# Performance work log

Hardware: AMD Instinct MI355X
Metric: run time of the kernel (lower is better)

## Reference

```python
import jax, jax.numpy as jnp
import numpy as np

B, IDF, RES = 32, 64, 128
CDF, SRC_L, A_DIM = 768, 18, 100
QUERY_L = RES * RES


def setup_inputs() -> dict:
    key = jax.random.key(0)
    ks = jax.random.split(key, 5)
    inputs = jax.random.normal(ks[0], (B, IDF, RES, RES), dtype=jnp.float32)
    context = jax.random.normal(ks[1], (B, CDF, SRC_L), dtype=jnp.float32)
    conv_ctx_w = jax.random.normal(ks[2], (IDF, CDF), dtype=jnp.float32) * (1.0 / np.sqrt(CDF))
    conv_w = jax.random.normal(ks[3], (IDF,), dtype=jnp.float32) * (1.0 / np.sqrt(IDF))
    conv_b = jnp.zeros((1,), dtype=jnp.float32)
    fc_w = jax.random.normal(ks[4], (A_DIM, QUERY_L), dtype=jnp.float32) * (1.0 / np.sqrt(QUERY_L))
    fc_b = jnp.zeros((A_DIM,), dtype=jnp.float32)
    return {"inputs": inputs, "context": context, "conv_ctx_w": conv_ctx_w,
            "conv_w": conv_w, "conv_b": conv_b, "fc_w": fc_w, "fc_b": fc_b}


def reference(inputs, context, conv_ctx_w, conv_w, conv_b, fc_w, fc_b):
    b, idf, ih, iw = inputs.shape
    queryL = ih * iw
    # target: [b, idf, queryL]
    target = inputs.reshape(b, idf, queryL)
    # 1x1 conv on context (conv_context): [b, idf, sourceL]
    sourceT = jnp.einsum('ic,bcs->bis', conv_ctx_w, context)
    # attn scores: [b, queryL, sourceL]; softmax over sourceL (dim=1 on flattened view)
    attn = jnp.einsum('biq,bis->bqs', target, sourceT)
    attn = jax.nn.softmax(attn, axis=-1)
    # weighted context: [b, idf, queryL]
    wctx = jnp.einsum('bis,bqs->biq', sourceT, attn)
    # 1x1 conv to single channel (self.conv): [b, queryL]
    wctx = jnp.einsum('i,biq->bq', conv_w, wctx) + conv_b
    # att_fc: [b, a_dim]
    out = wctx @ fc_w.T + fc_b
    return out
```

## Files before the change

### kernel.cpp

```cpp
#include <hip/hip_runtime.h>

#define BB 32
#define IDF 64
#define QL 16384
#define CDF 768
#define SL 18
#define SLP 20
#define ADIM 100

__device__ __forceinline__ void fma4(float4& a, const float4 v, const float s) {
    a.x += v.x * s; a.y += v.y * s; a.z += v.z * s; a.w += v.w * s;
}

__global__ __launch_bounds__(256, 2) void k1_source(
        const float* __restrict__ ctx,
        const float* __restrict__ wic,
        float* __restrict__ sT)
{
    __shared__ __align__(16) float ctx_l[CDF * SLP];
    const int b = blockIdx.x;
    const int g = blockIdx.y;
    const float* ctxb = ctx + (size_t)b * CDF * SL;

    for (int t = threadIdx.x; t < CDF * SL; t += 256) {
        const int c = t / SL;
        const int s = t - c * SL;
        ctx_l[c * SLP + s] = ctxb[t];
    }
    __syncthreads();

    const int wave = threadIdx.x >> 6;
    const int lane = threadIdx.x & 63;

    for (int ii = 0; ii < 4; ii++) {
        const int i = g * 16 + wave * 4 + ii;
        float acc[SL];
#pragma unroll
        for (int s = 0; s < SL; s++) acc[s] = 0.f;

        for (int k = 0; k < CDF / 64; k++) {
            const int c = k * 64 + lane;
            const float wv = wic[i * CDF + c];
            float r[SLP];
            const float4* r4 = (const float4*)&ctx_l[c * SLP];
            ((float4*)r)[0] = r4[0];
            ((float4*)r)[1] = r4[1];
            ((float4*)r)[2] = r4[2];
            ((float4*)r)[3] = r4[3];
            ((float4*)r)[4] = r4[4];
#pragma unroll
            for (int s = 0; s < SL; s++) acc[s] += wv * r[s];
        }
#pragma unroll
        for (int s = 0; s < SL; s++) {
            float a = acc[s];
#pragma unroll
            for (int off = 32; off; off >>= 1) a += __shfl_xor(a, off, 64);
            if (lane == 0) sT[((size_t)b * IDF + i) * SLP + s] = a;
        }
    }
}

__global__ __launch_bounds__(256, 2) void k2_attn(
        const float* __restrict__ inp,
        const float* __restrict__ sT,
        const float* __restrict__ conv_w,
        const float* __restrict__ conv_b,
        float* __restrict__ wq)
{
    __shared__ __align__(16) float st_l[IDF * SLP];
    __shared__ float cw_l[IDF];
    __shared__ float v_l[SL];
    const int b = blockIdx.y;
    const int tid = threadIdx.x;

    for (int t = tid; t < IDF * SLP; t += 256) st_l[t] = sT[(size_t)b * IDF * SLP + t];
    if (tid < IDF) cw_l[tid] = conv_w[tid];
    __syncthreads();
    if (tid < SL) {
        float a = 0.f;
#pragma unroll
        for (int i = 0; i < IDF; i++) a += cw_l[i] * st_l[i * SLP + tid];
        v_l[tid] = a;
    }
    __syncthreads();

    const int q = (blockIdx.x * 256 + tid) * 4;
    const float4* ip4 = (const float4*)(inp + (size_t)b * IDF * QL + q);

    float4 sc[SL];
#pragma unroll
    for (int s = 0; s < SL; s++) sc[s] = make_float4(0.f, 0.f, 0.f, 0.f);

#pragma unroll 4
    for (int i = 0; i < IDF; i++) {
        const float4 x = ip4[i * (QL / 4)];
        float r[SLP];
        const float4* r4 = (const float4*)&st_l[i * SLP];
        ((float4*)r)[0] = r4[0];
        ((float4*)r)[1] = r4[1];
        ((float4*)r)[2] = r4[2];
        ((float4*)r)[3] = r4[3];
        ((float4*)r)[4] = r4[4];
#pragma unroll
        for (int s = 0; s < SL; s++) fma4(sc[s], x, r[s]);
    }

    float4 m = sc[0];
#pragma unroll
    for (int s = 1; s < SL; s++) {
        m.x = fmaxf(m.x, sc[s].x); m.y = fmaxf(m.y, sc[s].y);
        m.z = fmaxf(m.z, sc[s].z); m.w = fmaxf(m.w, sc[s].w);
    }
    float4 l = make_float4(0.f, 0.f, 0.f, 0.f);
    float4 o = make_float4(0.f, 0.f, 0.f, 0.f);
#pragma unroll
    for (int s = 0; s < SL; s++) {
        const float vs = v_l[s];
        float4 p;
        p.x = __expf(sc[s].x - m.x); p.y = __expf(sc[s].y - m.y);
        p.z = __expf(sc[s].z - m.z); p.w = __expf(sc[s].w - m.w);
        l.x += p.x; l.y += p.y; l.z += p.z; l.w += p.w;
        o.x += p.x * vs; o.y += p.y * vs; o.z += p.z * vs; o.w += p.w * vs;
    }
    const float cb = conv_b[0];
    float4 res;
    res.x = o.x / l.x + cb; res.y = o.y / l.y + cb;
    res.z = o.z / l.z + cb; res.w = o.w / l.w + cb;
    ((float4*)(wq + (size_t)b * QL))[blockIdx.x * 256 + tid] = res;
}

__global__ __launch_bounds__(256) void k3a_init(const float* __restrict__ fc_b,
                                                float* __restrict__ out)
{
    const int idx = blockIdx.x * 256 + threadIdx.x;
    if (idx < BB * ADIM) out[idx] = fc_b[idx % ADIM];
}

__global__ __launch_bounds__(256) void k3_fc(
        const float* __restrict__ wq,
        const float* __restrict__ fcw,
        float* __restrict__ out)
{
    const int w = blockIdx.x * 4 + (threadIdx.x >> 6);
    const int lane = threadIdx.x & 63;
    const int b4 = w / 200;
    const int rem = w - b4 * 200;
    const int ag = rem >> 3;
    const int qc = rem & 7;
    const int b0 = b4 * 4, a0 = ag * 4, q0 = qc * 2048;

    float4 acc[4][4];
#pragma unroll
    for (int i = 0; i < 4; i++)
#pragma unroll
        for (int j = 0; j < 4; j++) acc[i][j] = make_float4(0.f, 0.f, 0.f, 0.f);

#pragma unroll 2
    for (int k = 0; k < 8; k++) {
        const int qi = q0 + (k * 64 + lane) * 4;
        float4 wv[4], fv[4];
#pragma unroll
        for (int i = 0; i < 4; i++) wv[i] = *(const float4*)(wq + (size_t)(b0 + i) * QL + qi);
#pragma unroll
        for (int j = 0; j < 4; j++) fv[j] = *(const float4*)(fcw + (size_t)(a0 + j) * QL + qi);
#pragma unroll
        for (int i = 0; i < 4; i++) {
#pragma unroll
            for (int j = 0; j < 4; j++) {
                acc[i][j].x += wv[i].x * fv[j].x;
                acc[i][j].y += wv[i].y * fv[j].y;
                acc[i][j].z += wv[i].z * fv[j].z;
                acc[i][j].w += wv[i].w * fv[j].w;
            }
        }
    }

#pragma unroll
    for (int i = 0; i < 4; i++) {
#pragma unroll
        for (int j = 0; j < 4; j++) {
            float r = acc[i][j].x + acc[i][j].y + acc[i][j].z + acc[i][j].w;
#pragma unroll
            for (int off = 32; off; off >>= 1) r += __shfl_xor(r, off, 64);
            if (lane == 0) atomicAdd(&out[(b0 + i) * ADIM + a0 + j], r);
        }
    }
}

extern "C" void kernel_launch(void* const* d_in, const int* in_sizes, int n_in,
                              void* d_out, int out_size, void* d_ws, size_t ws_size,
                              hipStream_t stream)
{
    const float* inputs     = (const float*)d_in[0];
    const float* context    = (const float*)d_in[1];
    const float* conv_ctx_w = (const float*)d_in[2];
    const float* conv_w     = (const float*)d_in[3];
    const float* conv_b     = (const float*)d_in[4];
    const float* fc_w       = (const float*)d_in[5];
    const float* fc_b       = (const float*)d_in[6];
    float* out = (float*)d_out;

    float* ws = (float*)d_ws;
    float* sT = ws;
    float* wq = ws + (size_t)BB * IDF * SLP;

    k1_source<<<dim3(BB, 4), dim3(256), 0, stream>>>(context, conv_ctx_w, sT);
    k2_attn<<<dim3(QL / 1024, BB), dim3(256), 0, stream>>>(inputs, sT, conv_w, conv_b, wq);
    k3a_init<<<dim3((BB * ADIM + 255) / 256), dim3(256), 0, stream>>>(fc_b, out);
    k3_fc<<<dim3(400), dim3(256), 0, stream>>>(wq, fc_w, out);
}
```

Baseline: 259.0 us.

## Batch output rows in source conv, fold bias init into FC kernel

```diff
diff --git a/kernel.cpp b/kernel.cpp
--- a/kernel.cpp
+++ b/kernel.cpp
@@ -31,32 +31,40 @@
 
     const int wave = threadIdx.x >> 6;
     const int lane = threadIdx.x & 63;
-
+    const int i0 = g * 16 + wave * 4;
+
+    float acc[4][SL];
+#pragma unroll
+    for (int ii = 0; ii < 4; ii++)
+#pragma unroll
+        for (int s = 0; s < SL; s++) acc[ii][s] = 0.f;
+
+    for (int k = 0; k < CDF / 64; k++) {
+        const int c = k * 64 + lane;
+        float wv[4];
+#pragma unroll
+        for (int ii = 0; ii < 4; ii++) wv[ii] = wic[(i0 + ii) * CDF + c];
+        float r[SLP];
+        const float4* r4 = (const float4*)&ctx_l[c * SLP];
+        ((float4*)r)[0] = r4[0];
+        ((float4*)r)[1] = r4[1];
+        ((float4*)r)[2] = r4[2];
+        ((float4*)r)[3] = r4[3];
+        ((float4*)r)[4] = r4[4];
+#pragma unroll
+        for (int ii = 0; ii < 4; ii++)
+#pragma unroll
+            for (int s = 0; s < SL; s++) acc[ii][s] += wv[ii] * r[s];
+    }
+
+#pragma unroll
     for (int ii = 0; ii < 4; ii++) {
-        const int i = g * 16 + wave * 4 + ii;
-        float acc[SL];
-#pragma unroll
-        for (int s = 0; s < SL; s++) acc[s] = 0.f;
-
-        for (int k = 0; k < CDF / 64; k++) {
-            const int c = k * 64 + lane;
-            const float wv = wic[i * CDF + c];
-            float r[SLP];
-            const float4* r4 = (const float4*)&ctx_l[c * SLP];
-            ((float4*)r)[0] = r4[0];
-            ((float4*)r)[1] = r4[1];
-            ((float4*)r)[2] = r4[2];
-            ((float4*)r)[3] = r4[3];
-            ((float4*)r)[4] = r4[4];
-#pragma unroll
-            for (int s = 0; s < SL; s++) acc[s] += wv * r[s];
-        }
 #pragma unroll
         for (int s = 0; s < SL; s++) {
-            float a = acc[s];
+            float a = acc[ii][s];
 #pragma unroll
             for (int off = 32; off; off >>= 1) a += __shfl_xor(a, off, 64);
-            if (lane == 0) sT[((size_t)b * IDF + i) * SLP + s] = a;
+            if (lane == 0) sT[((size_t)b * IDF + i0 + ii) * SLP + s] = a;
         }
     }
 }
@@ -92,7 +100,7 @@
 #pragma unroll
     for (int s = 0; s < SL; s++) sc[s] = make_float4(0.f, 0.f, 0.f, 0.f);
 
-#pragma unroll 4
+#pragma unroll 8
     for (int i = 0; i < IDF; i++) {
         const float4 x = ip4[i * (QL / 4)];
         float r[SLP];
@@ -130,25 +138,19 @@
     ((float4*)(wq + (size_t)b * QL))[blockIdx.x * 256 + tid] = res;
 }
 
-__global__ __launch_bounds__(256) void k3a_init(const float* __restrict__ fc_b,
-                                                float* __restrict__ out)
-{
-    const int idx = blockIdx.x * 256 + threadIdx.x;
-    if (idx < BB * ADIM) out[idx] = fc_b[idx % ADIM];
-}
-
-__global__ __launch_bounds__(256) void k3_fc(
+__global__ __launch_bounds__(256, 2) void k3_fc(
         const float* __restrict__ wq,
         const float* __restrict__ fcw,
+        const float* __restrict__ fc_b,
         float* __restrict__ out)
 {
-    const int w = blockIdx.x * 4 + (threadIdx.x >> 6);
+    __shared__ float part[4 * 16];
+    const int b4 = blockIdx.x / 25;
+    const int ag = blockIdx.x - b4 * 25;
+    const int b0 = b4 * 4, a0 = ag * 4;
+    const int wave = threadIdx.x >> 6;
     const int lane = threadIdx.x & 63;
-    const int b4 = w / 200;
-    const int rem = w - b4 * 200;
-    const int ag = rem >> 3;
-    const int qc = rem & 7;
-    const int b0 = b4 * 4, a0 = ag * 4, q0 = qc * 2048;
+    const int q0 = wave * 4096;
 
     float4 acc[4][4];
 #pragma unroll
@@ -157,7 +159,7 @@
         for (int j = 0; j < 4; j++) acc[i][j] = make_float4(0.f, 0.f, 0.f, 0.f);
 
 #pragma unroll 2
-    for (int k = 0; k < 8; k++) {
+    for (int k = 0; k < 16; k++) {
         const int qi = q0 + (k * 64 + lane) * 4;
         float4 wv[4], fv[4];
 #pragma unroll
@@ -183,8 +185,16 @@
             float r = acc[i][j].x + acc[i][j].y + acc[i][j].z + acc[i][j].w;
 #pragma unroll
             for (int off = 32; off; off >>= 1) r += __shfl_xor(r, off, 64);
-            if (lane == 0) atomicAdd(&out[(b0 + i) * ADIM + a0 + j], r);
+            if (lane == 0) part[wave * 16 + i * 4 + j] = r;
         }
+    }
+    __syncthreads();
+    if (threadIdx.x < 16) {
+        const int i = threadIdx.x >> 2;
+        const int j = threadIdx.x & 3;
+        const float s = part[threadIdx.x] + part[16 + threadIdx.x] +
+                        part[32 + threadIdx.x] + part[48 + threadIdx.x];
+        out[(b0 + i) * ADIM + a0 + j] = s + fc_b[a0 + j];
     }
 }
 
@@ -207,6 +217,5 @@
 
     k1_source<<<dim3(BB, 4), dim3(256), 0, stream>>>(context, conv_ctx_w, sT);
     k2_attn<<<dim3(QL / 1024, BB), dim3(256), 0, stream>>>(inputs, sT, conv_w, conv_b, wq);
-    k3a_init<<<dim3((BB * ADIM + 255) / 256), dim3(256), 0, stream>>>(fc_b, out);
-    k3_fc<<<dim3(400), dim3(256), 0, stream>>>(wq, fc_w, out);
-}
+    k3_fc<<<dim3(200), dim3(256), 0, stream>>>(wq, fc_w, fc_b, out);
+}
```

After: 273.3 us. 5.5% more time.
